# Kernel tuning notes

Measured on AMD Instinct MI355X. Metric: run time of the kernel, lower is better.

Reference implementation:

```python
import jax, jax.numpy as jnp
import numpy as np

N = 50000      # nodes
E = 800000     # edges
IN = 128       # input features (arxiv)
HID = 128      # hidden per head
HEADS = 3      # arxiv_data=True -> 3 heads
OUT = 40       # classes
EPS = 1e-5     # BN eps
SLOPE = 0.2    # DGL GATConv leaky_relu negative slope


def setup_inputs() -> dict:
    key = jax.random.key(0)
    ks = jax.random.split(key, 20)
    x = jax.random.normal(ks[0], (N, IN), jnp.float32)
    src = jax.random.randint(ks[1], (E,), 0, N, dtype=jnp.int32)
    # guarantee every node has >=1 in-edge so edge_softmax is well-defined
    dst = jnp.concatenate([jnp.arange(N, dtype=jnp.int32),
                           jax.random.randint(ks[2], (E - N,), 0, N, dtype=jnp.int32)])

    def lin(k, fi, fo):
        return jax.random.normal(k, (fi, fo), jnp.float32) * (1.0 / np.sqrt(fi))

    def attn(k, h, d):
        return jax.random.normal(k, (h, d), jnp.float32) * 0.1

    return {
        "x": x, "src": src, "dst": dst,
        # layer 0: IN -> HEADS*HID
        "W0": lin(ks[3], IN, HEADS * HID),
        "al0": attn(ks[4], HEADS, HID), "ar0": attn(ks[5], HEADS, HID),
        "b0": jnp.zeros((HEADS * HID,), jnp.float32),
        # layer 1: HEADS*HID -> HEADS*HID
        "W1": lin(ks[6], HEADS * HID, HEADS * HID),
        "al1": attn(ks[7], HEADS, HID), "ar1": attn(ks[8], HEADS, HID),
        "b1": jnp.zeros((HEADS * HID,), jnp.float32),
        # layer 2: HEADS*HID -> OUT, 1 head
        "W2": lin(ks[9], HEADS * HID, OUT),
        "al2": attn(ks[10], 1, OUT), "ar2": attn(ks[11], 1, OUT),
        "b2": jnp.zeros((OUT,), jnp.float32),
        # batch norms over HEADS*HID channels
        "g0": jnp.ones((HEADS * HID,), jnp.float32), "be0": jnp.zeros((HEADS * HID,), jnp.float32),
        "g1": jnp.ones((HEADS * HID,), jnp.float32), "be1": jnp.zeros((HEADS * HID,), jnp.float32),
    }


def gat_layer(h, src, dst, W, al, ar, b, heads, d_out):
    # fc + per-head split: [N, heads, d_out]
    f = (h @ W).reshape(-1, heads, d_out)
    el = jnp.einsum('nhd,hd->nh', f, al)          # [N, H]
    er = jnp.einsum('nhd,hd->nh', f, ar)          # [N, H]
    e = jax.nn.leaky_relu(el[src] + er[dst], SLOPE)  # [E, H]
    # edge softmax over incoming edges of each dst node
    m = jax.ops.segment_max(e, dst, num_segments=N)
    ex = jnp.exp(e - m[dst])
    s = jax.ops.segment_sum(ex, dst, num_segments=N)
    a = ex / s[dst]                                # [E, H]
    # u_mul_e + sum aggregation
    out = jax.ops.segment_sum(f[src] * a[:, :, None], dst, num_segments=N)  # [N, H, D]
    out = out + b.reshape(1, heads, d_out)
    return out.reshape(-1, heads * d_out)


def batch_norm(h, g, b):
    mu = h.mean(axis=0)
    var = h.var(axis=0)
    return g * (h - mu) / jnp.sqrt(var + EPS) + b


def reference(x, src, dst, W0, al0, ar0, b0, W1, al1, ar1, b1,
              W2, al2, ar2, b2, g0, be0, g1, be1):
    h = gat_layer(x, src, dst, W0, al0, ar0, b0, HEADS, HID)
    h = jax.nn.relu(batch_norm(h, g0, be0))        # dropout: eval mode (identity)
    h = gat_layer(h, src, dst, W1, al1, ar1, b1, HEADS, HID)
    h = jax.nn.relu(batch_norm(h, g1, be1))
    out = gat_layer(h, src, dst, W2, al2, ar2, b2, 1, OUT)
    return out
```

## Files before the change

### kernel.cpp

```cpp
#include <hip/hip_runtime.h>
#include <hip/hip_bf16.h>

typedef __hip_bfloat16 bf16;
typedef __attribute__((ext_vector_type(8))) short short8;
typedef __attribute__((ext_vector_type(4))) float f32x4;

static constexpr int N_NODES  = 50000;
static constexpr int N_EDGES  = 800000;
static constexpr int F_IN     = 128;
static constexpr int D_HID    = 128;
static constexpr int H_HEADS  = 3;
static constexpr int F_OUT    = 40;
static constexpr int DEG_CAP  = 128;
static constexpr float BN_EPS = 1e-5f;
static constexpr float SLOPE  = 0.2f;

__device__ __forceinline__ float bfLo(unsigned int u) { return __uint_as_float(u << 16); }
__device__ __forceinline__ float bfHi(unsigned int u) { return __uint_as_float(u & 0xffff0000u); }
__device__ __forceinline__ float bfs(unsigned short s) { return __uint_as_float(((unsigned int)s) << 16); }
__device__ __forceinline__ unsigned int packbf(float a, float b) {
  union { bf16 h[2]; unsigned int u; } pk;
  pk.h[0] = __float2bfloat16(a);
  pk.h[1] = __float2bfloat16(b);
  return pk.u;
}
__device__ __forceinline__ short f2bf_s(float v) {
  bf16 h = __float2bfloat16(v);
  union { bf16 b; short s; } c; c.b = h; return c.s;
}

__global__ __launch_bounds__(256) void gemm_mfma(const short* __restrict__ A,
                                                 const short* __restrict__ WT,
                                                 bf16* __restrict__ C,
                                                 const float* __restrict__ alp,
                                                 const float* __restrict__ arp,
                                                 float* __restrict__ el,
                                                 float* __restrict__ er,
                                                 const float* __restrict__ bnsrc,
                                                 const float* __restrict__ g,
                                                 const float* __restrict__ be,
                                                 float* __restrict__ bnstats,
                                                 int M, int K, int Nc, int els, int ers,
                                                 int lda, int ldc, int adiag) {
  constexpr int BM = 128, BN = 128, BK = 64, LDP = BK + 8;
  __shared__ short As[BM * LDP];
  __shared__ short Bs[BN * LDP];
  __shared__ float ecomb[128][4];
  __shared__ float sscale[384];
  __shared__ float sshift[384];
  int tid = threadIdx.x;
  int wave = tid >> 6, lane = tid & 63;
  int bm = blockIdx.y, bn = blockIdx.x;
  int m15 = lane & 15, quad = lane >> 4;
  int ksub = quad * 8;
  int wr = wave >> 1, wc = wave & 1;
  int srow = tid >> 3;
  int scol = (tid & 7) * 8;
  int acol0 = adiag ? bn * K : 0;

  if (bnsrc) {
    float inv_n = 1.f / (float)M;
    for (int c = tid; c < K; c += 256) {
      float mu = bnsrc[c] * inv_n;
      float var = bnsrc[K + c] * inv_n - mu * mu;
      float s = g[c] * rsqrtf(var + BN_EPS);
      sscale[c] = s;
      sshift[c] = be[c] - mu * s;
    }
    __syncthreads();
  }

  f32x4 acc[4][4];
#pragma unroll
  for (int i = 0; i < 4; ++i)
#pragma unroll
    for (int j = 0; j < 4; ++j) acc[i][j] = (f32x4){0.f, 0.f, 0.f, 0.f};

  for (int k0 = 0; k0 < K; k0 += BK) {
    int cb = k0 + scol;
    f32x4 sc0, sc1, sh0, sh1;
    if (bnsrc) {
      sc0 = *(const f32x4*)&sscale[cb]; sc1 = *(const f32x4*)&sscale[cb + 4];
      sh0 = *(const f32x4*)&sshift[cb]; sh1 = *(const f32x4*)&sshift[cb + 4];
    }
#pragma unroll
    for (int c = 0; c < 4; ++c) {
      int r = srow + c * 32;
      int gr = bm * BM + r; if (gr >= M) gr = M - 1;
      short8 av = *(const short8*)&A[(size_t)gr * lda + acol0 + k0 + scol];
      if (bnsrc) {
#pragma unroll
        for (int j = 0; j < 8; ++j) {
          float v = bfs((unsigned short)av[j]);
          float s = (j < 4) ? ((const float*)&sc0)[j] : ((const float*)&sc1)[j - 4];
          float t = (j < 4) ? ((const float*)&sh0)[j] : ((const float*)&sh1)[j - 4];
          float y = v * s + t;
          av[j] = f2bf_s(y > 0.f ? y : 0.f);
        }
      }
      *(short8*)&As[r * LDP + scol] = av;
      int gn = bn * BN + r;
      *(short8*)&Bs[r * LDP + scol] = *(const short8*)&WT[(size_t)gn * K + k0 + scol];
    }
    __syncthreads();
#pragma unroll
    for (int ks = 0; ks < BK; ks += 32) {
      short8 a[4], b[4];
#pragma unroll
      for (int i = 0; i < 4; ++i)
        a[i] = *(const short8*)&As[(wr * 64 + i * 16 + m15) * LDP + ks + ksub];
#pragma unroll
      for (int j = 0; j < 4; ++j)
        b[j] = *(const short8*)&Bs[(wc * 64 + j * 16 + m15) * LDP + ks + ksub];
#pragma unroll
      for (int i = 0; i < 4; ++i)
#pragma unroll
        for (int j = 0; j < 4; ++j)
          acc[i][j] = __builtin_amdgcn_mfma_f32_16x16x32_bf16(a[i], b[j], acc[i][j], 0, 0, 0);
    }
    __syncthreads();
  }

  int h = bn;
  float alv[4], arv[4];
#pragma unroll
  for (int j = 0; j < 4; ++j) {
    int col = bn * BN + wc * 64 + j * 16 + m15;
    alv[j] = alp[col];
    arv[j] = arp[col];
  }
  float csum[4] = {0.f, 0.f, 0.f, 0.f}, csq[4] = {0.f, 0.f, 0.f, 0.f};
#pragma unroll
  for (int i = 0; i < 4; ++i) {
#pragma unroll
    for (int r = 0; r < 4; ++r) {
      int rl = wr * 64 + i * 16 + quad * 4 + r;
      int row = bm * BM + rl;
      float pe = 0.f, pr = 0.f;
#pragma unroll
      for (int j = 0; j < 4; ++j) {
        float v = acc[i][j][r];
        pe += v * alv[j];
        pr += v * arv[j];
        if (bnstats && row < M) { csum[j] += v; csq[j] += v * v; }
        int col = bn * BN + wc * 64 + j * 16 + m15;
        if (row < M && col < Nc)
          C[(size_t)row * ldc + col] = __float2bfloat16(v);
      }
#pragma unroll
      for (int off = 1; off < 16; off <<= 1) {
        pe += __shfl_xor(pe, off);
        pr += __shfl_xor(pr, off);
      }
      if (m15 == 0) {
        ecomb[rl][wc] = pe;
        ecomb[rl][2 + wc] = pr;
      }
    }
  }
  if (bnstats) {
#pragma unroll
    for (int j = 0; j < 4; ++j) {
      csum[j] += __shfl_xor(csum[j], 16); csum[j] += __shfl_xor(csum[j], 32);
      csq[j]  += __shfl_xor(csq[j], 16);  csq[j]  += __shfl_xor(csq[j], 32);
    }
    if (quad == 0) {
#pragma unroll
      for (int j = 0; j < 4; ++j) {
        int col = bn * BN + wc * 64 + j * 16 + m15;
        atomicAdd(bnstats + col, csum[j]);
        atomicAdd(bnstats + Nc + col, csq[j]);
      }
    }
  }
  __syncthreads();
  if (tid < 128) {
    int row = bm * BM + tid;
    if (row < M) {
      el[(size_t)row * els + h] = ecomb[tid][0] + ecomb[tid][1];
      er[(size_t)row * ers + h] = ecomb[tid][2] + ecomb[tid][3];
    }
  }
}

__global__ void prep_kernel(const float* __restrict__ x, bf16* __restrict__ abuf,
                            const float* __restrict__ W0, const float* __restrict__ W1,
                            const float* __restrict__ W2, bf16* __restrict__ WT0,
                            bf16* __restrict__ WT1, bf16* __restrict__ WT2,
                            const float* __restrict__ al2, const float* __restrict__ ar2,
                            float* __restrict__ alp2, float* __restrict__ arp2,
                            int* __restrict__ fill, float* __restrict__ bnzero,
                            const float* __restrict__ al0, const float* __restrict__ ar0,
                            float* __restrict__ vl, float* __restrict__ vr) {
  const int NTOT = N_NODES * F_IN;
  for (int i = blockIdx.x * blockDim.x + threadIdx.x; i < NTOT;
       i += gridDim.x * blockDim.x) {
    abuf[i] = __float2bfloat16(x[i]);
    if (i < 384 * 384) { int n = i / 384, k = i - n * 384; WT1[i] = __float2bfloat16(W1[(size_t)k * 384 + n]); }
    if (i < 384 * 128) { int n = i / 128, k = i - n * 128; WT0[i] = __float2bfloat16(W0[(size_t)k * 384 + n]); }
    if (i < 128 * 384) { int n = i / 384, k = i - n * 384; WT2[i] = __float2bfloat16(n < F_OUT ? W2[(size_t)k * F_OUT + n] : 0.f); }
    if (i < N_NODES) fill[i] = 0;
    if (i < 4 * 384) bnzero[i] = 0.f;
    if (i < 128) { alp2[i] = i < F_OUT ? al2[i] : 0.f; arp2[i] = i < F_OUT ? ar2[i] : 0.f; }
  }
  if (blockIdx.x < 96) {
    int wid = blockIdx.x * 4 + (threadIdx.x >> 6);
    int lane = threadIdx.x & 63;
    int h = wid >> 7, k = wid & 127;
    const float2* wrow = (const float2*)(W0 + (size_t)k * 384 + h * 128);
    const float2* av = (const float2*)(al0 + h * 128);
    const float2* rv = (const float2*)(ar0 + h * 128);
    float2 wv = wrow[lane], a2 = av[lane], r2 = rv[lane];
    float sl = wv.x * a2.x + wv.y * a2.y;
    float sr = wv.x * r2.x + wv.y * r2.y;
#pragma unroll
    for (int off = 32; off > 0; off >>= 1) {
      sl += __shfl_xor(sl, off);
      sr += __shfl_xor(sr, off);
    }
    if (lane == 0) { vl[wid] = sl; vr[wid] = sr; }
  }
}

__global__ void bucket_kernel(const int* __restrict__ src, const int* __restrict__ dst,
                              int* __restrict__ fill, int* __restrict__ bucket, int E) {
  int i = blockIdx.x * blockDim.x + threadIdx.x;
  if (i < E) {
    int d = dst[i];
    int pos = atomicAdd(fill + d, 1);
    if (pos < DEG_CAP) bucket[(size_t)d * DEG_CAP + pos] = src[i];
  }
}

__global__ __launch_bounds__(256) void elr_kernel(const unsigned int* __restrict__ x2,
                                                  const float* __restrict__ vl,
                                                  const float* __restrict__ vr,
                                                  float* __restrict__ el,
                                                  float* __restrict__ er, int N) {
  int wv = threadIdx.x >> 6, lane = threadIdx.x & 63;
  int n = blockIdx.x * 4 + wv;
  if (n >= N) return;
  unsigned int u = x2[(size_t)n * 64 + lane];
  float v0 = bfLo(u), v1 = bfHi(u);
  float pl[3], pr[3];
#pragma unroll
  for (int h = 0; h < 3; ++h) {
    float2 a2 = *(const float2*)&vl[h * 128 + 2 * lane];
    float2 r2 = *(const float2*)&vr[h * 128 + 2 * lane];
    pl[h] = v0 * a2.x + v1 * a2.y;
    pr[h] = v0 * r2.x + v1 * r2.y;
  }
#pragma unroll
  for (int h = 0; h < 3; ++h) {
#pragma unroll
    for (int off = 32; off > 0; off >>= 1) {
      pl[h] += __shfl_xor(pl[h], off);
      pr[h] += __shfl_xor(pr[h], off);
    }
  }
  if (lane == 0) {
    *(float4*)&el[(size_t)n * 4] = make_float4(pl[0], pl[1], pl[2], 0.f);
    er[(size_t)n * 3 + 0] = pr[0];
    er[(size_t)n * 3 + 1] = pr[1];
    er[(size_t)n * 3 + 2] = pr[2];
  }
}

__global__ __launch_bounds__(256) void aggr_x_kernel(
    const int* __restrict__ fill, const int* __restrict__ bucket,
    const float4* __restrict__ el4, const float* __restrict__ er,
    const uint4* __restrict__ xq, uint4* __restrict__ outq, int N) {
  __shared__ float wls[4][64 * 3];
  __shared__ int   sls[4][64];
  int wv = threadIdx.x >> 6;
  int d = (blockIdx.x * 256 + threadIdx.x) >> 6;
  int lane = threadIdx.x & 63;
  if (d >= N) return;
  int deg = fill[d]; if (deg > DEG_CAP) deg = DEG_CAP;
  const int* myb = bucket + (size_t)d * DEG_CAP;
  float* mywls = wls[wv];
  int* mysls = sls[wv];
  int g = lane >> 4;
  int cch = lane & 15;

  float erd[3];
#pragma unroll
  for (int h = 0; h < 3; ++h) erd[h] = er[d * 3 + h];
  float acc[3][8];
#pragma unroll
  for (int h = 0; h < 3; ++h)
#pragma unroll
    for (int j = 0; j < 8; ++j) acc[h][j] = 0.f;
  float sp[3] = {0.f, 0.f, 0.f};

  for (int k0 = 0; k0 < deg; k0 += 64) {
    int nk = deg - k0; if (nk > 64) nk = 64;
    if (lane < nk) {
      int s_l = myb[k0 + lane];
      mysls[lane] = s_l;
      float4 e4 = el4[s_l];
      float ev[3] = {e4.x, e4.y, e4.z};
#pragma unroll
      for (int h = 0; h < 3; ++h) {
        float sc = ev[h] + erd[h];
        sc = sc > 0.f ? sc : SLOPE * sc;
        float w = __expf(sc);
        mywls[lane * 3 + h] = w;
        sp[h] += w;
      }
    }
    for (int e0 = 0; e0 < nk; e0 += 4) {
      int e = e0 + g;
      if (e < nk) {
        int se = mysls[e];
        float w0s = mywls[e * 3], w1s = mywls[e * 3 + 1], w2s = mywls[e * 3 + 2];
        uint4 u = xq[(size_t)se * 16 + cch];
        float ff[8] = {bfLo(u.x), bfHi(u.x), bfLo(u.y), bfHi(u.y),
                       bfLo(u.z), bfHi(u.z), bfLo(u.w), bfHi(u.w)};
#pragma unroll
        for (int j = 0; j < 8; ++j) {
          acc[0][j] += w0s * ff[j];
          acc[1][j] += w1s * ff[j];
          acc[2][j] += w2s * ff[j];
        }
      }
    }
  }
#pragma unroll
  for (int h = 0; h < 3; ++h) {
#pragma unroll
    for (int off = 32; off > 0; off >>= 1) sp[h] += __shfl_xor(sp[h], off);
  }
#pragma unroll
  for (int h = 0; h < 3; ++h)
#pragma unroll
    for (int j = 0; j < 8; ++j) {
      acc[h][j] += __shfl_xor(acc[h][j], 16);
      acc[h][j] += __shfl_xor(acc[h][j], 32);
    }
  if (g < 3) {
    float og[8];
#pragma unroll
    for (int j = 0; j < 8; ++j)
      og[j] = (g == 0) ? acc[0][j] : (g == 1) ? acc[1][j] : acc[2][j];
    float spg = (g == 0) ? sp[0] : (g == 1) ? sp[1] : sp[2];
    float inv = 1.f / spg;
    uint4 r;
    r.x = packbf(og[0] * inv, og[1] * inv);
    r.y = packbf(og[2] * inv, og[3] * inv);
    r.z = packbf(og[4] * inv, og[5] * inv);
    r.w = packbf(og[6] * inv, og[7] * inv);
    outq[(size_t)d * 48 + g * 16 + cch] = r;
  }
}

template <int H, int D>
__global__ __launch_bounds__(256) void aggr_fused_kernel(
    const int* __restrict__ fill, const int* __restrict__ bucket,
    const float4* __restrict__ el4, const float* __restrict__ er,
    const bf16* __restrict__ f, uint4* __restrict__ outq, int N) {
  constexpr int W = H * D / 2;
  constexpr int WQ = W / 4;
  __shared__ float wls[4][64 * H];
  int wv = threadIdx.x >> 6;
  int d = (blockIdx.x * 256 + threadIdx.x) >> 6;
  int lane = threadIdx.x & 63;
  if (d >= N) return;
  int deg = fill[d]; if (deg > DEG_CAP) deg = DEG_CAP;
  const int* myb = bucket + (size_t)d * DEG_CAP;
  const uint4* fq = (const uint4*)f;
  float* mywls = wls[wv];
  int hsel = lane >> 4;

  float erd[H];
#pragma unroll
  for (int h = 0; h < H; ++h) erd[h] = er[d * H + h];
  float acc[8];
#pragma unroll
  for (int j = 0; j < 8; ++j) acc[j] = 0.f;
  float sp[H];
#pragma unroll
  for (int h = 0; h < H; ++h) sp[h] = 0.f;

  for (int k0 = 0; k0 < deg; k0 += 64) {
    int nk = deg - k0; if (nk > 64) nk = 64;
    int s_l = 0;
    if (lane < nk) {
      s_l = myb[k0 + lane];
      float4 e4 = el4[s_l];
      float ev[3] = {e4.x, e4.y, e4.z};
#pragma unroll
      for (int h = 0; h < H; ++h) {
        float sc = ev[h] + erd[h];
        sc = sc > 0.f ? sc : SLOPE * sc;
        float w = __expf(sc);
        mywls[lane * H + h] = w;
        sp[h] += w;
      }
    }
    for (int e = 0; e < nk; ++e) {
      int se = __shfl(s_l, e);
      if (lane < WQ) {
        float w = mywls[e * H + hsel];
        uint4 u = fq[(size_t)se * WQ + lane];
        acc[0] += w * bfLo(u.x); acc[1] += w * bfHi(u.x);
        acc[2] += w * bfLo(u.y); acc[3] += w * bfHi(u.y);
        acc[4] += w * bfLo(u.z); acc[5] += w * bfHi(u.z);
        acc[6] += w * bfLo(u.w); acc[7] += w * bfHi(u.w);
      }
    }
  }
#pragma unroll
  for (int h = 0; h < H; ++h) {
#pragma unroll
    for (int off = 32; off > 0; off >>= 1) sp[h] += __shfl_xor(sp[h], off);
  }
  if (lane < WQ) {
    float inv = 1.f / sp[hsel];
    uint4 r;
    r.x = packbf(acc[0] * inv, acc[1] * inv);
    r.y = packbf(acc[2] * inv, acc[3] * inv);
    r.z = packbf(acc[4] * inv, acc[5] * inv);
    r.w = packbf(acc[6] * inv, acc[7] * inv);
    outq[(size_t)d * WQ + lane] = r;
  }
}

__global__ __launch_bounds__(256) void aggr_out_kernel(
    const int* __restrict__ fill, const int* __restrict__ bucket,
    const float* __restrict__ el, const float* __restrict__ er,
    const bf16* __restrict__ f, const float* __restrict__ bias,
    float* __restrict__ out, int N) {
  constexpr int DW = F_OUT / 2;
  constexpr int LDW = 32;
  __shared__ float wls[4][64];
  __shared__ int   sls[4][64];
  int wv = threadIdx.x >> 6;
  int d = (blockIdx.x * 256 + threadIdx.x) >> 6;
  int lane = threadIdx.x & 63;
  if (d >= N) return;
  int deg = fill[d]; if (deg > DEG_CAP) deg = DEG_CAP;
  const int* myb = bucket + (size_t)d * DEG_CAP;
  const unsigned int* fu = (const unsigned int*)f;
  float* mywls = wls[wv];
  int* mysls = sls[wv];
  int g = lane / DW;
  int cch = lane - g * DW;
  float erd = er[d];
  float a0 = 0.f, a1 = 0.f, sp = 0.f;
  for (int k0 = 0; k0 < deg; k0 += 64) {
    int nk = deg - k0; if (nk > 64) nk = 64;
    if (lane < nk) {
      int s_l = myb[k0 + lane];
      mysls[lane] = s_l;
      float sc = el[s_l] + erd;
      sc = sc > 0.f ? sc : SLOPE * sc;
      float w = __expf(sc);
      mywls[lane] = w;
      sp += w;
    }
    for (int e0 = 0; e0 < nk; e0 += 3) {
      int e = e0 + g;
      if (g < 3 && e < nk) {
        int se = mysls[e];
        float w = mywls[e];
        unsigned int u = fu[(size_t)se * LDW + cch];
        a0 += w * bfLo(u);
        a1 += w * bfHi(u);
      }
    }
  }
#pragma unroll
  for (int off = 32; off > 0; off >>= 1) sp += __shfl_xor(sp, off);
  float b0 = __shfl(a0, (lane + DW) & 63), b1 = __shfl(a1, (lane + DW) & 63);
  float c0 = __shfl(a0, (lane + 2 * DW) & 63), c1 = __shfl(a1, (lane + 2 * DW) & 63);
  if (lane < DW) {
    float inv = 1.f / sp;
    float o0 = (a0 + b0 + c0) * inv + bias[2 * lane];
    float o1 = (a1 + b1 + c1) * inv + bias[2 * lane + 1];
    *(float2*)&out[(size_t)d * F_OUT + 2 * lane] = make_float2(o0, o1);
  }
}

__global__ void bn_stats_kernel(const unsigned int* __restrict__ h2, float* __restrict__ sum,
                                float* __restrict__ sumsq, int N, int C2) {
  int c = threadIdx.x;
  int step = gridDim.x;
  float s0 = 0.f, q0 = 0.f, s1 = 0.f, q1 = 0.f;
  int n = blockIdx.x;
  for (; n + 3 * step < N; n += 4 * step) {
    unsigned int ua = h2[(size_t)n * C2 + c];
    unsigned int ub = h2[(size_t)(n + step) * C2 + c];
    unsigned int uc = h2[(size_t)(n + 2 * step) * C2 + c];
    unsigned int ud = h2[(size_t)(n + 3 * step) * C2 + c];
    float va0 = bfLo(ua), va1 = bfHi(ua);
    float vb0 = bfLo(ub), vb1 = bfHi(ub);
    float vc0 = bfLo(uc), vc1 = bfHi(uc);
    float vd0 = bfLo(ud), vd1 = bfHi(ud);
    s0 += va0 + vb0 + vc0 + vd0;
    s1 += va1 + vb1 + vc1 + vd1;
    q0 += va0 * va0 + vb0 * vb0 + vc0 * vc0 + vd0 * vd0;
    q1 += va1 * va1 + vb1 * vb1 + vc1 * vc1 + vd1 * vd1;
  }
  for (; n < N; n += step) {
    unsigned int u = h2[(size_t)n * C2 + c];
    float v0 = bfLo(u), v1 = bfHi(u);
    s0 += v0; q0 += v0 * v0;
    s1 += v1; q1 += v1 * v1;
  }
  atomicAdd(sum + 2 * c, s0);
  atomicAdd(sum + 2 * c + 1, s1);
  atomicAdd(sumsq + 2 * c, q0);
  atomicAdd(sumsq + 2 * c + 1, q1);
}

static inline int cdiv(int a, int b) { return (a + b - 1) / b; }

extern "C" void kernel_launch(void* const* d_in, const int* in_sizes, int n_in,
                              void* d_out, int out_size, void* d_ws, size_t ws_size,
                              hipStream_t stream) {
  const float* x   = (const float*)d_in[0];
  const int* src   = (const int*)d_in[1];
  const int* dst   = (const int*)d_in[2];
  const float* W0  = (const float*)d_in[3];
  const float* al0 = (const float*)d_in[4];
  const float* ar0 = (const float*)d_in[5];
  const float* W1  = (const float*)d_in[7];
  const float* al1 = (const float*)d_in[8];
  const float* ar1 = (const float*)d_in[9];
  const float* W2  = (const float*)d_in[11];
  const float* al2 = (const float*)d_in[12];
  const float* ar2 = (const float*)d_in[13];
  const float* b2  = (const float*)d_in[14];
  const float* g0  = (const float*)d_in[15];
  const float* be0 = (const float*)d_in[16];
  const float* g1  = (const float*)d_in[17];
  const float* be1 = (const float*)d_in[18];
  float* out = (float*)d_out;

  const int N = N_NODES, E = N_EDGES, H = H_HEADS;
  const int C = H * D_HID;

  char* p = (char*)d_ws;
  auto take = [&](size_t bytes) {
    char* r = p;
    p += (bytes + 255) & ~(size_t)255;
    return r;
  };
  bf16*   f_buf   = (bf16*) take((size_t)N * C * sizeof(bf16));
  bf16*   hbuf    = (bf16*) take((size_t)N * C * sizeof(bf16));
  bf16*   abuf    = (bf16*) take((size_t)N * C * sizeof(bf16));
  float*  elbuf   = (float*)take((size_t)N * 4 * sizeof(float));
  float*  er      = (float*)take((size_t)N * H * sizeof(float));
  float*  bnbuf   = (float*)take((size_t)4 * C * sizeof(float));
  bf16*   WT0     = (bf16*) take((size_t)C * F_IN * sizeof(bf16));
  bf16*   WT1     = (bf16*) take((size_t)C * C * sizeof(bf16));
  bf16*   WT2     = (bf16*) take((size_t)128 * C * sizeof(bf16));
  float*  alp2    = (float*)take(128 * sizeof(float));
  float*  arp2    = (float*)take(128 * sizeof(float));
  float*  vlbuf   = (float*)take(384 * sizeof(float));
  float*  vrbuf   = (float*)take(384 * sizeof(float));
  int*    fill    = (int*)take((size_t)N * sizeof(int));
  int*    bucket  = (int*)take((size_t)N * DEG_CAP * sizeof(int));
  float*  bnA = bnbuf;
  float*  bnB = bnbuf + 2 * C;

  prep_kernel<<<cdiv(N * F_IN, 256), 256, 0, stream>>>(x, abuf, W0, W1, W2, WT0, WT1, WT2,
                                                       al2, ar2, alp2, arp2, fill, bnbuf,
                                                       al0, ar0, vlbuf, vrbuf);
  bucket_kernel<<<cdiv(E, 256), 256, 0, stream>>>(src, dst, fill, bucket, E);
  elr_kernel<<<cdiv(N, 4), 256, 0, stream>>>((const unsigned int*)abuf, vlbuf, vrbuf,
                                             elbuf, er, N);

  aggr_x_kernel<<<cdiv(N * 64, 256), 256, 0, stream>>>(
      fill, bucket, (const float4*)elbuf, er, (const uint4*)abuf,
      (uint4*)f_buf, N);
  gemm_mfma<<<dim3(3, cdiv(N, 128)), 256, 0, stream>>>(
      (const short*)f_buf, (const short*)WT0, hbuf, al0, ar0, elbuf, er,
      nullptr, nullptr, nullptr, bnA, N, F_IN, C, 4, 3, C, C, 1);

  gemm_mfma<<<dim3(C / 128, cdiv(N, 128)), 256, 0, stream>>>(
      (const short*)hbuf, (const short*)WT1, f_buf, al1, ar1, elbuf, er,
      bnA, g0, be0, nullptr, N, C, C, 4, 3, C, C, 0);
  aggr_fused_kernel<H_HEADS, D_HID><<<cdiv(N * 64, 256), 256, 0, stream>>>(
      fill, bucket, (const float4*)elbuf, er, f_buf, (uint4*)hbuf, N);
  bn_stats_kernel<<<1024, C / 2, 0, stream>>>((const unsigned int*)hbuf, bnB, bnB + C, N, C / 2);

  gemm_mfma<<<dim3(1, cdiv(N, 128)), 256, 0, stream>>>(
      (const short*)hbuf, (const short*)WT2, f_buf, alp2, arp2, elbuf, er,
      bnB, g1, be1, nullptr, N, C, F_OUT, 1, 1, C, 64, 0);
  aggr_out_kernel<<<cdiv(N * 64, 256), 256, 0, stream>>>(
      fill, bucket, elbuf, er, f_buf, b2, out, N);
}
```

Before: 513.9 us.

## Split layer-1 aggregation into weight precompute and channel-chunked gather passes

The layer-1 GEMM now writes features in a chunk-major layout (32-column chunks). A new kernel computes normalized attention weights once per edge and packs each one as fp16 with the source index. A chunked aggregation kernel then gathers each 64-byte chunk across 12 passes, which is meant to improve cache locality over gathering full 768-byte rows. The change also folds edge bucketing into elr_kernel, lowers DEG_CAP to 64 and drops the multi-chunk degree loops. The risks are that nodes with more than 64 in-edges are silently truncated, fp16 weights lose precision, and the 16-bit source index packing cannot represent node IDs of 65536 or more.

After: 662.6 us. +28.9%, slower.

```diff
diff --git a/kernel.cpp b/kernel.cpp
--- a/kernel.cpp
+++ b/kernel.cpp
@@ -1,5 +1,6 @@
 #include <hip/hip_runtime.h>
 #include <hip/hip_bf16.h>
+#include <hip/hip_fp16.h>
 
 typedef __hip_bfloat16 bf16;
 typedef __attribute__((ext_vector_type(8))) short short8;
@@ -11,7 +12,8 @@
 static constexpr int D_HID    = 128;
 static constexpr int H_HEADS  = 3;
 static constexpr int F_OUT    = 40;
-static constexpr int DEG_CAP  = 128;
+static constexpr int DEG_CAP  = 64;
+static constexpr int CHUNKS   = 12;
 static constexpr float BN_EPS = 1e-5f;
 static constexpr float SLOPE  = 0.2f;
 
@@ -41,7 +43,7 @@
                                                  const float* __restrict__ be,
                                                  float* __restrict__ bnstats,
                                                  int M, int K, int Nc, int els, int ers,
-                                                 int lda, int ldc, int adiag) {
+                                                 int lda, int ldc, int adiag, int cchunk) {
   constexpr int BM = 128, BN = 128, BK = 64, LDP = BK + 8;
   __shared__ short As[BM * LDP];
   __shared__ short Bs[BN * LDP];
@@ -144,8 +146,12 @@
         pr += v * arv[j];
         if (bnstats && row < M) { csum[j] += v; csq[j] += v * v; }
         int col = bn * BN + wc * 64 + j * 16 + m15;
-        if (row < M && col < Nc)
-          C[(size_t)row * ldc + col] = __float2bfloat16(v);
+        if (row < M && col < Nc) {
+          size_t addr = cchunk
+              ? ((size_t)((col >> 5) * N_NODES + row) * 32 + (col & 31))
+              : ((size_t)row * ldc + col);
+          C[addr] = __float2bfloat16(v);
+        }
       }
 #pragma unroll
       for (int off = 1; off < 16; off <<= 1) {
@@ -222,21 +228,22 @@
   }
 }
 
-__global__ void bucket_kernel(const int* __restrict__ src, const int* __restrict__ dst,
-                              int* __restrict__ fill, int* __restrict__ bucket, int E) {
-  int i = blockIdx.x * blockDim.x + threadIdx.x;
-  if (i < E) {
-    int d = dst[i];
-    int pos = atomicAdd(fill + d, 1);
-    if (pos < DEG_CAP) bucket[(size_t)d * DEG_CAP + pos] = src[i];
-  }
-}
-
 __global__ __launch_bounds__(256) void elr_kernel(const unsigned int* __restrict__ x2,
                                                   const float* __restrict__ vl,
                                                   const float* __restrict__ vr,
                                                   float* __restrict__ el,
-                                                  float* __restrict__ er, int N) {
+                                                  float* __restrict__ er,
+                                                  const int* __restrict__ src,
+                                                  const int* __restrict__ dst,
+                                                  int* __restrict__ fill,
+                                                  int* __restrict__ bucket,
+                                                  int N, int E) {
+  int gid = blockIdx.x * 256 + threadIdx.x;
+  if (gid < E) {
+    int d = dst[gid];
+    int pos = atomicAdd(fill + d, 1);
+    if (pos < DEG_CAP) bucket[(size_t)d * DEG_CAP + pos] = src[gid];
+  }
   int wv = threadIdx.x >> 6, lane = threadIdx.x & 63;
   int n = blockIdx.x * 4 + wv;
   if (n >= N) return;
@@ -293,10 +300,10 @@
     for (int j = 0; j < 8; ++j) acc[h][j] = 0.f;
   float sp[3] = {0.f, 0.f, 0.f};
 
-  for (int k0 = 0; k0 < deg; k0 += 64) {
-    int nk = deg - k0; if (nk > 64) nk = 64;
+  {
+    int nk = deg;
     if (lane < nk) {
-      int s_l = myb[k0 + lane];
+      int s_l = myb[lane];
       mysls[lane] = s_l;
       float4 e4 = el4[s_l];
       float ev[3] = {e4.x, e4.y, e4.z};
@@ -354,76 +361,78 @@
   }
 }
 
-template <int H, int D>
-__global__ __launch_bounds__(256) void aggr_fused_kernel(
+__global__ __launch_bounds__(256) void wgt_kernel(
     const int* __restrict__ fill, const int* __restrict__ bucket,
     const float4* __restrict__ el4, const float* __restrict__ er,
-    const bf16* __restrict__ f, uint4* __restrict__ outq, int N) {
-  constexpr int W = H * D / 2;
-  constexpr int WQ = W / 4;
-  __shared__ float wls[4][64 * H];
-  int wv = threadIdx.x >> 6;
+    unsigned int* __restrict__ ew, int N) {
   int d = (blockIdx.x * 256 + threadIdx.x) >> 6;
   int lane = threadIdx.x & 63;
   if (d >= N) return;
   int deg = fill[d]; if (deg > DEG_CAP) deg = DEG_CAP;
-  const int* myb = bucket + (size_t)d * DEG_CAP;
-  const uint4* fq = (const uint4*)f;
-  float* mywls = wls[wv];
-  int hsel = lane >> 4;
-
-  float erd[H];
-#pragma unroll
-  for (int h = 0; h < H; ++h) erd[h] = er[d * H + h];
-  float acc[8];
-#pragma unroll
-  for (int j = 0; j < 8; ++j) acc[j] = 0.f;
-  float sp[H];
-#pragma unroll
-  for (int h = 0; h < H; ++h) sp[h] = 0.f;
-
-  for (int k0 = 0; k0 < deg; k0 += 64) {
-    int nk = deg - k0; if (nk > 64) nk = 64;
-    int s_l = 0;
-    if (lane < nk) {
-      s_l = myb[k0 + lane];
-      float4 e4 = el4[s_l];
-      float ev[3] = {e4.x, e4.y, e4.z};
-#pragma unroll
-      for (int h = 0; h < H; ++h) {
-        float sc = ev[h] + erd[h];
-        sc = sc > 0.f ? sc : SLOPE * sc;
-        float w = __expf(sc);
-        mywls[lane * H + h] = w;
-        sp[h] += w;
-      }
-    }
-    for (int e = 0; e < nk; ++e) {
-      int se = __shfl(s_l, e);
-      if (lane < WQ) {
-        float w = mywls[e * H + hsel];
-        uint4 u = fq[(size_t)se * WQ + lane];
-        acc[0] += w * bfLo(u.x); acc[1] += w * bfHi(u.x);
-        acc[2] += w * bfLo(u.y); acc[3] += w * bfHi(u.y);
-        acc[4] += w * bfLo(u.z); acc[5] += w * bfHi(u.z);
-        acc[6] += w * bfLo(u.w); acc[7] += w * bfHi(u.w);
-      }
-    }
-  }
-#pragma unroll
-  for (int h = 0; h < H; ++h) {
+  float erd[3];
+#pragma unroll
+  for (int h = 0; h < 3; ++h) erd[h] = er[d * 3 + h];
+  float w[3] = {0.f, 0.f, 0.f};
+  int s_l = 0;
+  if (lane < deg) {
+    s_l = bucket[(size_t)d * DEG_CAP + lane];
+    float4 e4 = el4[s_l];
+    float ev[3] = {e4.x, e4.y, e4.z};
+#pragma unroll
+    for (int h = 0; h < 3; ++h) {
+      float sc = ev[h] + erd[h];
+      sc = sc > 0.f ? sc : SLOPE * sc;
+      w[h] = __expf(sc);
+    }
+  }
+  float sp[3] = {w[0], w[1], w[2]};
+#pragma unroll
+  for (int h = 0; h < 3; ++h) {
 #pragma unroll
     for (int off = 32; off > 0; off >>= 1) sp[h] += __shfl_xor(sp[h], off);
   }
-  if (lane < WQ) {
-    float inv = 1.f / sp[hsel];
-    uint4 r;
-    r.x = packbf(acc[0] * inv, acc[1] * inv);
-    r.y = packbf(acc[2] * inv, acc[3] * inv);
-    r.z = packbf(acc[4] * inv, acc[5] * inv);
-    r.w = packbf(acc[6] * inv, acc[7] * inv);
-    outq[(size_t)d * WQ + lane] = r;
-  }
+  if (lane < deg) {
+    unsigned int sbits = ((unsigned int)s_l) << 16;
+#pragma unroll
+    for (int h = 0; h < 3; ++h) {
+      unsigned short wb = __half_as_ushort(__float2half(w[h] / sp[h]));
+      ew[(size_t)h * N * DEG_CAP + (size_t)d * DEG_CAP + lane] = sbits | (unsigned int)wb;
+    }
+  }
+}
+
+__global__ __launch_bounds__(256) void aggr_pass_kernel(
+    const int* __restrict__ fill, const unsigned int* __restrict__ ew,
+    const unsigned int* __restrict__ fc, unsigned int* __restrict__ outw, int N) {
+  int nb = (N + 3) >> 2;
+  int ch = blockIdx.x / nb;
+  int db = blockIdx.x - ch * nb;
+  int wv = threadIdx.x >> 6, lane = threadIdx.x & 63;
+  int d = db * 4 + wv;
+  if (d >= N) return;
+  int h = ch >> 2;
+  int deg = fill[d]; if (deg > DEG_CAP) deg = DEG_CAP;
+  unsigned int ewv = 0;
+  if (lane < deg) ewv = ew[(size_t)h * N * DEG_CAP + (size_t)d * DEG_CAP + lane];
+  int cch = lane & 15;
+  int g = lane >> 4;
+  const unsigned int* fcc = fc + (size_t)ch * N * 16;
+  float a0 = 0.f, a1 = 0.f;
+  for (int e0 = 0; e0 < deg; e0 += 4) {
+    int e = e0 + g;
+    int esafe = e < deg ? e : 0;
+    unsigned int pk = __shfl(ewv, esafe);
+    if (e < deg) {
+      float w = __half2float(__ushort_as_half((unsigned short)(pk & 0xffffu)));
+      int se = pk >> 16;
+      unsigned int u = fcc[(size_t)se * 16 + cch];
+      a0 += w * bfLo(u);
+      a1 += w * bfHi(u);
+    }
+  }
+  a0 += __shfl_xor(a0, 16); a0 += __shfl_xor(a0, 32);
+  a1 += __shfl_xor(a1, 16); a1 += __shfl_xor(a1, 32);
+  if (g == 0) outw[(size_t)d * 192 + ch * 16 + cch] = packbf(a0, a1);
 }
 
 __global__ __launch_bounds__(256) void aggr_out_kernel(
@@ -448,10 +457,10 @@
   int cch = lane - g * DW;
   float erd = er[d];
   float a0 = 0.f, a1 = 0.f, sp = 0.f;
-  for (int k0 = 0; k0 < deg; k0 += 64) {
-    int nk = deg - k0; if (nk > 64) nk = 64;
+  {
+    int nk = deg;
     if (lane < nk) {
-      int s_l = myb[k0 + lane];
+      int s_l = myb[lane];
       mysls[lane] = s_l;
       float sc = el[s_l] + erd;
       sc = sc > 0.f ? sc : SLOPE * sc;
@@ -562,33 +571,36 @@
   float*  vrbuf   = (float*)take(384 * sizeof(float));
   int*    fill    = (int*)take((size_t)N * sizeof(int));
   int*    bucket  = (int*)take((size_t)N * DEG_CAP * sizeof(int));
+  bf16*   f2buf   = (bf16*) take((size_t)N * 64 * sizeof(bf16));
   float*  bnA = bnbuf;
   float*  bnB = bnbuf + 2 * C;
+  unsigned int* ew = (unsigned int*)abuf;
 
   prep_kernel<<<cdiv(N * F_IN, 256), 256, 0, stream>>>(x, abuf, W0, W1, W2, WT0, WT1, WT2,
                                                        al2, ar2, alp2, arp2, fill, bnbuf,
                                                        al0, ar0, vlbuf, vrbuf);
-  bucket_kernel<<<cdiv(E, 256), 256, 0, stream>>>(src, dst, fill, bucket, E);
   elr_kernel<<<cdiv(N, 4), 256, 0, stream>>>((const unsigned int*)abuf, vlbuf, vrbuf,
-                                             elbuf, er, N);
+                                             elbuf, er, src, dst, fill, bucket, N, E);
 
   aggr_x_kernel<<<cdiv(N * 64, 256), 256, 0, stream>>>(
       fill, bucket, (const float4*)elbuf, er, (const uint4*)abuf,
       (uint4*)f_buf, N);
   gemm_mfma<<<dim3(3, cdiv(N, 128)), 256, 0, stream>>>(
       (const short*)f_buf, (const short*)WT0, hbuf, al0, ar0, elbuf, er,
-      nullptr, nullptr, nullptr, bnA, N, F_IN, C, 4, 3, C, C, 1);
+      nullptr, nullptr, nullptr, bnA, N, F_IN, C, 4, 3, C, C, 1, 0);
 
   gemm_mfma<<<dim3(C / 128, cdiv(N, 128)), 256, 0, stream>>>(
       (const short*)hbuf, (const short*)WT1, f_buf, al1, ar1, elbuf, er,
-      bnA, g0, be0, nullptr, N, C, C, 4, 3, C, C, 0);
-  aggr_fused_kernel<H_HEADS, D_HID><<<cdiv(N * 64, 256), 256, 0, stream>>>(
-      fill, bucket, (const float4*)elbuf, er, f_buf, (uint4*)hbuf, N);
+      bnA, g0, be0, nullptr, N, C, C, 4, 3, C, C, 0, 1);
+  wgt_kernel<<<cdiv(N * 64, 256), 256, 0, stream>>>(
+      fill, bucket, (const float4*)elbuf, er, ew, N);
+  aggr_pass_kernel<<<CHUNKS * cdiv(N, 4), 256, 0, stream>>>(
+      fill, ew, (const unsigned int*)f_buf, (unsigned int*)hbuf, N);
   bn_stats_kernel<<<1024, C / 2, 0, stream>>>((const unsigned int*)hbuf, bnB, bnB + C, N, C / 2);
 
   gemm_mfma<<<dim3(1, cdiv(N, 128)), 256, 0, stream>>>(
-      (const short*)hbuf, (const short*)WT2, f_buf, alp2, arp2, elbuf, er,
-      bnB, g1, be1, nullptr, N, C, F_OUT, 1, 1, C, 64, 0);
+      (const short*)hbuf, (const short*)WT2, f2buf, alp2, arp2, elbuf, er,
+      bnB, g1, be1, nullptr, N, C, F_OUT, 1, 1, C, 64, 0, 0);
   aggr_out_kernel<<<cdiv(N * 64, 256), 256, 0, stream>>>(
-      fill, bucket, elbuf, er, f_buf, b2, out, N);
-}
+      fill, bucket, elbuf, er, f2buf, b2, out, N);
+}
```
